# Kernel optimization log

Measured on AMD Instinct MI355X. Metric: run time of the kernel, lower is better.

Reference implementation:

```python
import jax, jax.numpy as jnp
import numpy as np

B, T, H, V = 16, 128, 512, 50257


def setup_inputs() -> dict:
    key = jax.random.key(0)
    ks = jax.random.split(key, 6)
    s = 0.05  # init_scale
    return {
        "tokens": jax.random.randint(ks[0], (B, T), 0, V, dtype=jnp.int32),
        "labels": jax.random.randint(ks[1], (B, T), 0, V, dtype=jnp.int32),
        "embedding": jax.random.normal(ks[2], (V, H), jnp.float32) * s,
        "W1": jax.random.normal(ks[3], (2 * H, 4 * H), jnp.float32) * s,
        "b1": jnp.zeros((4 * H,), jnp.float32),
        "W2": jax.random.normal(ks[4], (2 * H, 4 * H), jnp.float32) * s,
        "b2": jnp.zeros((4 * H,), jnp.float32),
        "softmax_w": jax.random.normal(ks[5], (H, V), jnp.float32) * s,
        "softmax_b": jnp.zeros((V,), jnp.float32),
    }


def _lstm_cell(x, h, c, W, b):
    # TF LSTMCell gate order: i, j (candidate), f, o; forget_bias = 0.0
    z = jnp.concatenate([x, h], axis=-1) @ W + b  # [B, 4H]
    i, j, f, o = jnp.split(z, 4, axis=-1)
    c_new = c * jax.nn.sigmoid(f) + jax.nn.sigmoid(i) * jnp.tanh(j)
    h_new = jnp.tanh(c_new) * jax.nn.sigmoid(o)
    return h_new, c_new


def _forward(tokens, labels, embedding, W1, b1, W2, b2, softmax_w, softmax_b):
    x = embedding[tokens]                 # [B, T, H] embedding lookup
    xs = jnp.swapaxes(x, 0, 1)            # [T, B, H] time-major for scan
    zeros = jnp.zeros((B, H), x.dtype)

    def step(carry, xt):
        c1, h1, c2, h2 = carry
        h1n, c1n = _lstm_cell(xt, h1, c1, W1, b1)
        h2n, c2n = _lstm_cell(h1n, h2, c2, W2, b2)
        return (c1n, h1n, c2n, h2n), h2n

    _, hs = jax.lax.scan(step, (zeros, zeros, zeros, zeros), xs)  # hs: [T, B, H]
    output = jnp.swapaxes(hs, 0, 1).reshape(-1, H)                # [B*T, H]
    logits = output @ softmax_w + softmax_b                       # [B*T, V]
    logp = jax.nn.log_softmax(logits, axis=-1)
    ll = jnp.take_along_axis(logp, labels.reshape(-1, 1), axis=1)[:, 0]
    cost = -jnp.sum(ll) / B  # sequence_loss_by_example summed, / batch_size
    return cost


def reference(tokens, labels, embedding, W1, b1, W2, b2, softmax_w, softmax_b):
    return _forward(tokens, labels, embedding, W1, b1, W2, b2, softmax_w, softmax_b)
```

## Files before the change

kernel.cpp:

```cpp
#include <hip/hip_runtime.h>

#define B_ 16
#define T_ 128
#define H_ 512
#define V_ 50257
#define VP_ 50304
#define NBLK 393
#define M_ (B_*T_)
#define N4H 2048
#define KH 512
#define NKB 16
#define FP_ 32
#define NTILES (NBLK * 16)
#define NWORK 224
#define NCHUNK (VP_ * 16 / 16)
#define HP_ 520

typedef __attribute__((ext_vector_type(8))) short short8;
typedef __attribute__((ext_vector_type(4))) float floatx4;
typedef unsigned long long u64;

static __device__ __forceinline__ unsigned short f2bf(float f) {
    unsigned int u = __builtin_bit_cast(unsigned int, f);
    unsigned int r = (u + 0x7FFFu + ((u >> 16) & 1u)) >> 16;
    return (unsigned short)r;
}
static __device__ __forceinline__ void st_ic(u64* p, u64 v) {
    __hip_atomic_store(p, v, __ATOMIC_RELAXED, __HIP_MEMORY_SCOPE_AGENT);
}

__global__ void k_init(const int* __restrict__ labels, int* __restrict__ lab_r,
                       unsigned short* __restrict__ zeroh, int* __restrict__ flags) {
    int tid = blockIdx.x * blockDim.x + threadIdx.x;
    if (tid < M_) {
        int t = tid >> 4, b = tid & 15;
        lab_r[tid] = labels[b * T_ + t];
    }
    if (tid < B_ * H_) zeroh[tid] = 0;
    if (tid < 34 * FP_) flags[tid] = 0;
}

__global__ void k_embed(const int* __restrict__ tokens, const float* __restrict__ emb,
                        unsigned short* __restrict__ X) {
    int tid = blockIdx.x * blockDim.x + threadIdx.x;
    if (tid >= M_ * H_) return;
    int row = tid >> 9, col = tid & 511;
    int t = row >> 4, b = row & 15;
    int tok = tokens[b * T_ + t];
    X[tid] = f2bf(emb[(size_t)tok * H_ + col]);
}

__global__ void k_pack(const float* __restrict__ src, int ld, int nvalid, int nkb,
                       int nchunks, unsigned short* __restrict__ dst) {
    int tid = blockIdx.x * blockDim.x + threadIdx.x;
    int lane = tid & 63, chunk = tid >> 6;
    if (chunk >= nchunks) return;
    int nt = chunk / nkb, kb = chunk % nkb;
    int n = nt * 16 + (lane & 15);
    int k = kb * 32 + ((lane >> 4) << 3);
    unsigned short vals[8];
    if (n < nvalid) {
#pragma unroll
        for (int j = 0; j < 8; ++j) vals[j] = f2bf(src[(size_t)(k + j) * ld + n]);
    } else {
#pragma unroll
        for (int j = 0; j < 8; ++j) vals[j] = 0;
    }
    *(short8*)(dst + (size_t)chunk * 512 + lane * 8) = *(short8*)vals;
}

__global__ __launch_bounds__(256, 2) void k_gemm_bias(
        const unsigned short* __restrict__ A, const unsigned short* __restrict__ Bp,
        const float* __restrict__ bias, float* __restrict__ C) {
    int bn = blockIdx.x, bm = blockIdx.y;
    int tid = threadIdx.x, lane = tid & 63, w = tid >> 6;
    int wm = w >> 1, wn = w & 1;
    int l15 = lane & 15, quad = lane >> 4;
    floatx4 acc[4][4];
#pragma unroll
    for (int i = 0; i < 4; ++i)
#pragma unroll
        for (int j = 0; j < 4; ++j) acc[i][j] = (floatx4){0.f, 0.f, 0.f, 0.f};
    const unsigned short* Abase = A + (size_t)(bm * 128 + wm * 64 + l15) * KH + quad * 8;
    int ntg0 = bn * 8 + wn * 4;
#pragma unroll 4
    for (int kb = 0; kb < NKB; ++kb) {
        short8 af[4], bf[4];
#pragma unroll
        for (int mt = 0; mt < 4; ++mt) af[mt] = *(const short8*)(Abase + mt * 16 * KH + kb * 32);
#pragma unroll
        for (int nt = 0; nt < 4; ++nt)
            bf[nt] = *(const short8*)(Bp + ((size_t)(ntg0 + nt) * NKB + kb) * 512 + lane * 8);
#pragma unroll
        for (int mt = 0; mt < 4; ++mt)
#pragma unroll
            for (int nt = 0; nt < 4; ++nt)
                acc[mt][nt] = __builtin_amdgcn_mfma_f32_16x16x32_bf16(af[mt], bf[nt], acc[mt][nt], 0, 0, 0);
    }
#pragma unroll
    for (int nt = 0; nt < 4; ++nt) {
        int col = bn * 128 + wn * 64 + nt * 16 + l15;
        float bv = bias[col];
#pragma unroll
        for (int mt = 0; mt < 4; ++mt) {
            int row0 = bm * 128 + wm * 64 + mt * 16 + quad * 4;
#pragma unroll
            for (int r = 0; r < 4; ++r)
                C[(size_t)(row0 + r) * N4H + col] = acc[mt][nt][r] + bv;
        }
    }
}

__global__ __launch_bounds__(512, 2) void k_mega(
        const float* __restrict__ Zpre1, const float* __restrict__ W1,
        const float* __restrict__ W2, const float* __restrict__ b2,
        const unsigned short* __restrict__ zeroh,
        unsigned short* __restrict__ H1, unsigned short* __restrict__ H2,
        int* __restrict__ flags,
        const float* __restrict__ sw, unsigned short* __restrict__ SWP,
        const float* __restrict__ sb, const int* __restrict__ lab_r,
        float* __restrict__ pm, float* __restrict__ ps, float* __restrict__ labv) {
    const int blk = blockIdx.x, tid = threadIdx.x;
    const int lane = tid & 63, w = tid >> 6;
    const int l15 = lane & 15, quad = lane >> 4;
    __shared__ unsigned short hs1[16 * HP_];
    __shared__ unsigned short hs2[16 * HP_];
    __shared__ float zs[128 * 17];
    u64* H1u = (u64*)H1;
    u64* H2u = (u64*)H2;

    if (blk < 32) {
        const bool isL2 = blk >= 16;
        const int bj = isL2 ? blk - 16 : blk;
        const int g = w >> 1, half = w & 1;
        const int nt = g * 32 + bj * 2 + half;
        const int colg = g * 512 + bj * 32 + half * 16 + l15;

        short8 bfr[32];
        {
            unsigned short vals[8];
            if (!isL2) {
#pragma unroll
                for (int kb = 0; kb < 16; ++kb) {
#pragma unroll
                    for (int j = 0; j < 8; ++j)
                        vals[j] = f2bf(W1[(size_t)(512 + kb * 32 + quad * 8 + j) * N4H + nt * 16 + l15]);
                    bfr[kb] = *(short8*)vals;
                }
            } else {
#pragma unroll
                for (int kb = 0; kb < 32; ++kb) {
#pragma unroll
                    for (int j = 0; j < 8; ++j)
                        vals[j] = f2bf(W2[(size_t)(kb * 32 + quad * 8 + j) * N4H + nt * 16 + l15]);
                    bfr[kb] = *(short8*)vals;
                }
            }
        }
        const float b2c = isL2 ? b2[colg] : 0.f;
        float creg = 0.f;

        for (int s = 0; s < T_; ++s) {
            float zpre[4];
            if (!isL2) {
#pragma unroll
                for (int r = 0; r < 4; ++r)
                    zpre[r] = Zpre1[(size_t)(s * 16 + quad * 4 + r) * N4H + colg];
            }
            if (w == 0 && (s > 0 || isL2)) {
                int tgt = 0x80000000;
                int* fp = flags;
                if (!isL2) {
                    if (lane < 16) { fp = flags + lane * FP_; tgt = s; }
                } else {
                    if (lane < 16) { fp = flags + lane * FP_; tgt = s + 1; }
                    else if (lane < 32) { fp = flags + lane * FP_; tgt = s; }
                }
                bool act = (!isL2 && lane < 16) || (isL2 && lane < 32);
                while (true) {
                    int v = act ? __hip_atomic_load(fp, __ATOMIC_RELAXED, __HIP_MEMORY_SCOPE_AGENT)
                                : 0x7fffffff;
                    if (__all(v >= tgt)) break;
                    __builtin_amdgcn_s_sleep(1);
                }
            }
            __syncthreads();

            if (!isL2) {
                const short8* src = (const short8*)((s == 0) ? zeroh
                                       : H1 + (size_t)(s - 1) * B_ * H_);
#pragma unroll
                for (int j = 0; j < 2; ++j) {
                    int idx = j * 512 + tid;
                    short8 v = src[idx];
                    *(short8*)(&hs1[(idx >> 6) * HP_ + (idx & 63) * 8]) = v;
                }
            } else {
                const short8* s1 = (const short8*)(H1 + (size_t)s * B_ * H_);
                const short8* s2 = (const short8*)((s == 0) ? zeroh
                                       : H2 + (size_t)(s - 1) * B_ * H_);
#pragma unroll
                for (int j = 0; j < 2; ++j) {
                    int idx = j * 512 + tid;
                    short8 v = s1[idx];
                    *(short8*)(&hs1[(idx >> 6) * HP_ + (idx & 63) * 8]) = v;
                }
#pragma unroll
                for (int j = 0; j < 2; ++j) {
                    int idx = j * 512 + tid;
                    short8 v = s2[idx];
                    *(short8*)(&hs2[(idx >> 6) * HP_ + (idx & 63) * 8]) = v;
                }
            }
            __syncthreads();

            if (!isL2) {
                floatx4 a0 = (floatx4){0.f,0.f,0.f,0.f}, a1 = (floatx4){0.f,0.f,0.f,0.f};
#pragma unroll
                for (int kb = 0; kb < 8; ++kb) {
                    short8 af = *(const short8*)(&hs1[l15 * HP_ + kb * 32 + quad * 8]);
                    a0 = __builtin_amdgcn_mfma_f32_16x16x32_bf16(af, bfr[kb], a0, 0, 0, 0);
                }
#pragma unroll
                for (int kb = 8; kb < 16; ++kb) {
                    short8 af = *(const short8*)(&hs1[l15 * HP_ + kb * 32 + quad * 8]);
                    a1 = __builtin_amdgcn_mfma_f32_16x16x32_bf16(af, bfr[kb], a1, 0, 0, 0);
                }
                const int zcol = g * 32 + half * 16 + l15;
#pragma unroll
                for (int r = 0; r < 4; ++r)
                    zs[zcol * 17 + quad * 4 + r] = a0[r] + a1[r] + zpre[r];
            } else {
                floatx4 a0 = (floatx4){0.f,0.f,0.f,0.f}, a1 = (floatx4){0.f,0.f,0.f,0.f};
#pragma unroll
                for (int kb = 0; kb < 16; ++kb) {
                    short8 af = *(const short8*)(&hs1[l15 * HP_ + kb * 32 + quad * 8]);
                    a0 = __builtin_amdgcn_mfma_f32_16x16x32_bf16(af, bfr[kb], a0, 0, 0, 0);
                }
#pragma unroll
                for (int kb = 0; kb < 16; ++kb) {
                    short8 af = *(const short8*)(&hs2[l15 * HP_ + kb * 32 + quad * 8]);
                    a1 = __builtin_amdgcn_mfma_f32_16x16x32_bf16(af, bfr[16 + kb], a1, 0, 0, 0);
                }
                const int zcol = g * 32 + half * 16 + l15;
#pragma unroll
                for (int r = 0; r < 4; ++r)
                    zs[zcol * 17 + quad * 4 + r] = a0[r] + a1[r] + b2c;
            }
            __syncthreads();

            {
                int u = tid >> 4, b = tid & 15;
                float zi = zs[(0 * 32 + u) * 17 + b];
                float zj = zs[(1 * 32 + u) * 17 + b];
                float zf = zs[(2 * 32 + u) * 17 + b];
                float zo = zs[(3 * 32 + u) * 17 + b];
                float si = 1.f / (1.f + __expf(-zi));
                float sf = 1.f / (1.f + __expf(-zf));
                float so = 1.f / (1.f + __expf(-zo));
                float cn = creg * sf + si * tanhf(zj);
                creg = cn;
                int hvi = (int)f2bf(tanhf(cn) * so);
                int lb = lane & 15;
                unsigned int h0 = (unsigned int)__shfl(hvi, lb);
                unsigned int h1v = (unsigned int)__shfl(hvi, lb + 16);
                unsigned int h2v = (unsigned int)__shfl(hvi, lb + 32);
                unsigned int h3v = (unsigned int)__shfl(hvi, lb + 48);
                if (lane < 16) {
                    u64 v = (u64)(h0 | (h1v << 16)) | ((u64)(h2v | (h3v << 16)) << 32);
                    u64* Hd = isL2 ? H2u : H1u;
                    st_ic(Hd + (size_t)(s * 16 + lane) * 128 + bj * 8 + w, v);
                }
            }
            __builtin_amdgcn_s_waitcnt(0x0F70);
            __syncthreads();
            if (tid == 0)
                __hip_atomic_store(flags + blk * FP_, s + 1, __ATOMIC_RELAXED,
                                   __HIP_MEMORY_SCOPE_AGENT);
        }
    } else {
        const int wid = blk - 32;
        int* wdone = flags + 32 * FP_;

        for (int t = 0; ; ++t) {
            int c = wid + NWORK * (8 * t + w);
            if (c >= NCHUNK) break;
            int cnt = c >> 4, ckb = c & 15;
            int n = cnt * 16 + l15;
            int kk = ckb * 32 + quad * 8;
            unsigned short vals[8];
            if (n < V_) {
#pragma unroll
                for (int j = 0; j < 8; ++j) vals[j] = f2bf(sw[(size_t)(kk + j) * V_ + n]);
            } else {
#pragma unroll
                for (int j = 0; j < 8; ++j) vals[j] = 0;
            }
            u64 v0 = (u64)vals[0] | ((u64)vals[1] << 16) | ((u64)vals[2] << 32) | ((u64)vals[3] << 48);
            u64 v1 = (u64)vals[4] | ((u64)vals[5] << 16) | ((u64)vals[6] << 32) | ((u64)vals[7] << 48);
            u64* dst = (u64*)(SWP + (size_t)c * 512 + lane * 8);
            st_ic(dst, v0);
            st_ic(dst + 1, v1);
        }
        __builtin_amdgcn_s_waitcnt(0x0F70);
        __syncthreads();
        if (tid == 0)
            __hip_atomic_fetch_add(wdone, 1, __ATOMIC_RELAXED, __HIP_MEMORY_SCOPE_AGENT);
        if (w == 0) {
            while (true) {
                int v = (lane == 0)
                    ? __hip_atomic_load(wdone, __ATOMIC_RELAXED, __HIP_MEMORY_SCOPE_AGENT)
                    : 0x7fffffff;
                if (__all(v >= NWORK)) break;
                __builtin_amdgcn_s_sleep(8);
            }
        }
        __syncthreads();

        int done_seen = 0;
        for (int k = wid; k < NTILES; k += NWORK) {
            int bm = k / NBLK, bn = k - bm * NBLK;
            int tgt = bm * 8 + 8;
            if (tgt > done_seen) {
                if (w == 0) {
                    int* fp = flags + (16 + (lane & 15)) * FP_;
                    while (true) {
                        int v = (lane < 16)
                            ? __hip_atomic_load(fp, __ATOMIC_RELAXED, __HIP_MEMORY_SCOPE_AGENT)
                            : 0x7fffffff;
                        if (__all(v >= tgt)) break;
                        __builtin_amdgcn_s_sleep(8);
                    }
                }
                __syncthreads();
                done_seen = tgt;
            }
            floatx4 acc[8];
#pragma unroll
            for (int j = 0; j < 8; ++j) acc[j] = (floatx4){0.f, 0.f, 0.f, 0.f};
            const short8* Abase = (const short8*)(H2 + (size_t)(bm * 128 + w * 16 + l15) * KH) + quad;
            int ntg0 = bn * 8;
#pragma unroll 4
            for (int kb = 0; kb < NKB; ++kb) {
                short8 af = Abase[kb * 4];
#pragma unroll
                for (int nt = 0; nt < 8; ++nt) {
                    short8 bf = *(const short8*)(SWP + ((size_t)(ntg0 + nt) * NKB + kb) * 512 + lane * 8);
                    acc[nt] = __builtin_amdgcn_mfma_f32_16x16x32_bf16(af, bf, acc[nt], 0, 0, 0);
                }
            }
            float bv[8]; int colg[8]; bool valid[8];
#pragma unroll
            for (int nt = 0; nt < 8; ++nt) {
                colg[nt] = bn * 128 + nt * 16 + l15;
                valid[nt] = colg[nt] < V_;
                bv[nt] = valid[nt] ? sb[colg[nt]] : 0.f;
            }
#pragma unroll
            for (int r = 0; r < 4; ++r) {
                float m = -3.0e38f;
#pragma unroll
                for (int nt = 0; nt < 8; ++nt) {
                    float v = valid[nt] ? acc[nt][r] + bv[nt] : -3.0e38f;
                    acc[nt][r] = v;
                    m = fmaxf(m, v);
                }
#pragma unroll
                for (int d = 1; d < 16; d <<= 1) m = fmaxf(m, __shfl_xor(m, d, 16));
                float sm = 0.f;
#pragma unroll
                for (int nt = 0; nt < 8; ++nt)
                    if (valid[nt]) sm += __expf(acc[nt][r] - m);
#pragma unroll
                for (int d = 1; d < 16; d <<= 1) sm += __shfl_xor(sm, d, 16);
                int rowg = bm * 128 + w * 16 + quad * 4 + r;
                int lc = lab_r[rowg];
#pragma unroll
                for (int nt = 0; nt < 8; ++nt)
                    if (valid[nt] && colg[nt] == lc) labv[rowg] = acc[nt][r];
                if (l15 == 0) {
                    pm[(size_t)rowg * NBLK + bn] = m;
                    ps[(size_t)rowg * NBLK + bn] = sm;
                }
            }
        }
    }
}

__global__ void k_rowreduce(const float* __restrict__ pm, const float* __restrict__ ps,
                            const float* __restrict__ labv, float* __restrict__ ll) {
    int row = blockIdx.x;
    int lane = threadIdx.x;
    const float* pmr = pm + (size_t)row * NBLK;
    const float* psr = ps + (size_t)row * NBLK;
    float m = -3.0e38f;
    for (int j = lane; j < NBLK; j += 64) m = fmaxf(m, pmr[j]);
#pragma unroll
    for (int d = 1; d < 64; d <<= 1) m = fmaxf(m, __shfl_xor(m, d, 64));
    float s = 0.f;
    for (int j = lane; j < NBLK; j += 64) s += psr[j] * __expf(pmr[j] - m);
#pragma unroll
    for (int d = 1; d < 64; d <<= 1) s += __shfl_xor(s, d, 64);
    if (lane == 0) ll[row] = labv[row] - m - logf(s);
}

__global__ void k_final(const float* __restrict__ ll, float* __restrict__ out) {
    int lane = threadIdx.x;
    float s = 0.f;
    for (int i = lane; i < M_; i += 64) s += ll[i];
#pragma unroll
    for (int d = 1; d < 64; d <<= 1) s += __shfl_xor(s, d, 64);
    if (lane == 0) out[0] = -s / (float)B_;
}

extern "C" void kernel_launch(void* const* d_in, const int* in_sizes, int n_in,
                              void* d_out, int out_size, void* d_ws, size_t ws_size,
                              hipStream_t stream) {
    const int* tokens = (const int*)d_in[0];
    const int* labels = (const int*)d_in[1];
    const float* emb = (const float*)d_in[2];
    const float* W1 = (const float*)d_in[3];
    const float* b1 = (const float*)d_in[4];
    const float* W2 = (const float*)d_in[5];
    const float* b2 = (const float*)d_in[6];
    const float* sw = (const float*)d_in[7];
    const float* sb = (const float*)d_in[8];
    float* out = (float*)d_out;

    char* ws = (char*)d_ws;
    size_t off = 0;
    auto alloc = [&](size_t bytes) {
        void* p = ws + off;
        off = (off + bytes + 255) & ~(size_t)255;
        return p;
    };
    unsigned short* X    = (unsigned short*)alloc((size_t)M_ * KH * 2);
    unsigned short* H1   = (unsigned short*)alloc((size_t)M_ * KH * 2);
    unsigned short* H2   = (unsigned short*)alloc((size_t)M_ * KH * 2);
    unsigned short* W1xP = (unsigned short*)alloc((size_t)N4H * KH * 2);
    unsigned short* SWP  = (unsigned short*)alloc((size_t)VP_ * KH * 2);
    float* Z     = (float*)alloc((size_t)M_ * N4H * 4);
    unsigned short* zeroh = (unsigned short*)alloc((size_t)B_ * H_ * 2);
    float* pm   = (float*)alloc((size_t)M_ * NBLK * 4);
    float* ps   = (float*)alloc((size_t)M_ * NBLK * 4);
    float* labv = (float*)alloc((size_t)M_ * 4);
    int*   lab_r = (int*)alloc((size_t)M_ * 4);
    float* ll   = (float*)alloc((size_t)M_ * 4);
    int*   flags = (int*)alloc((size_t)34 * FP_ * 4);

    k_init<<<64, 256, 0, stream>>>(labels, lab_r, zeroh, flags);
    k_embed<<<(M_ * H_) / 256, 256, 0, stream>>>(tokens, emb, X);
    k_pack<<<512, 256, 0, stream>>>(W1, N4H, N4H, 16, 2048, W1xP);

    k_gemm_bias<<<dim3(16, 16), 256, 0, stream>>>(X, W1xP, b1, Z);

    k_mega<<<256, 512, 0, stream>>>(Z, W1, W2, b2, zeroh, H1, H2, flags,
                                    sw, SWP, sb, lab_r, pm, ps, labv);

    k_rowreduce<<<M_, 64, 0, stream>>>(pm, ps, labv, ll);
    k_final<<<1, 64, 0, stream>>>(ll, out);
}
```

Measured before the change: 767.5 us.

## Replace flag barriers with step-tagged hidden-state words polled directly

Each hidden-state value is now stored as a 32-bit word that packs the bf16 value with a step tag. Consumer blocks poll their own slice of that data with cache-bypassing vector loads until every tag matches, which removes the separate flag write, the waitcnt-plus-barrier before signalling, and the flag poll on each recurrent step. Layer 2 keeps a double-buffered tagged slot and writes a flag only every 8 steps, for the downstream softmax workers. The step-0 matmuls are skipped and the three setup kernels are merged into one launch. In exchange, hidden-state traffic doubles and correctness now depends on the per-word tags, and therefore on stores landing atomically with their tags.

```diff
diff --git a/kernel.cpp b/kernel.cpp
--- a/kernel.cpp
+++ b/kernel.cpp
@@ -14,11 +14,13 @@
 #define NTILES (NBLK * 16)
 #define NWORK 224
 #define NCHUNK (VP_ * 16 / 16)
-#define HP_ 520
+#define HP_ 536
 
 typedef __attribute__((ext_vector_type(8))) short short8;
 typedef __attribute__((ext_vector_type(4))) float floatx4;
+typedef __attribute__((ext_vector_type(4))) unsigned int u32x4;
 typedef unsigned long long u64;
+typedef unsigned int u32;
 
 static __device__ __forceinline__ unsigned short f2bf(float f) {
     unsigned int u = __builtin_bit_cast(unsigned int, f);
@@ -28,45 +30,117 @@
 static __device__ __forceinline__ void st_ic(u64* p, u64 v) {
     __hip_atomic_store(p, v, __ATOMIC_RELAXED, __HIP_MEMORY_SCOPE_AGENT);
 }
-
-__global__ void k_init(const int* __restrict__ labels, int* __restrict__ lab_r,
-                       unsigned short* __restrict__ zeroh, int* __restrict__ flags) {
-    int tid = blockIdx.x * blockDim.x + threadIdx.x;
-    if (tid < M_) {
-        int t = tid >> 4, b = tid & 15;
-        lab_r[tid] = labels[b * T_ + t];
-    }
-    if (tid < B_ * H_) zeroh[tid] = 0;
-    if (tid < 34 * FP_) flags[tid] = 0;
-}
-
-__global__ void k_embed(const int* __restrict__ tokens, const float* __restrict__ emb,
-                        unsigned short* __restrict__ X) {
-    int tid = blockIdx.x * blockDim.x + threadIdx.x;
-    if (tid >= M_ * H_) return;
-    int row = tid >> 9, col = tid & 511;
-    int t = row >> 4, b = row & 15;
-    int tok = tokens[b * T_ + t];
-    X[tid] = f2bf(emb[(size_t)tok * H_ + col]);
-}
-
-__global__ void k_pack(const float* __restrict__ src, int ld, int nvalid, int nkb,
-                       int nchunks, unsigned short* __restrict__ dst) {
-    int tid = blockIdx.x * blockDim.x + threadIdx.x;
-    int lane = tid & 63, chunk = tid >> 6;
-    if (chunk >= nchunks) return;
-    int nt = chunk / nkb, kb = chunk % nkb;
-    int n = nt * 16 + (lane & 15);
-    int k = kb * 32 + ((lane >> 4) << 3);
-    unsigned short vals[8];
-    if (n < nvalid) {
-#pragma unroll
-        for (int j = 0; j < 8; ++j) vals[j] = f2bf(src[(size_t)(k + j) * ld + n]);
+static __device__ __forceinline__ void st_ic32(u32* p, u32 v) {
+    __hip_atomic_store(p, v, __ATOMIC_RELAXED, __HIP_MEMORY_SCOPE_AGENT);
+}
+
+static __device__ __forceinline__ void poll16(const u32* p, u32 tag, u32* v) {
+    u32x4 a0, a1, a2, a3;
+    while (true) {
+        asm volatile(
+            "global_load_dwordx4 %0, %4, off sc0 sc1\n\t"
+            "global_load_dwordx4 %1, %4, off offset:16 sc0 sc1\n\t"
+            "global_load_dwordx4 %2, %4, off offset:32 sc0 sc1\n\t"
+            "global_load_dwordx4 %3, %4, off offset:48 sc0 sc1\n\t"
+            "s_waitcnt vmcnt(0)"
+            : "=&v"(a0), "=&v"(a1), "=&v"(a2), "=&v"(a3)
+            : "v"(p)
+            : "memory");
+        u32 bad = 0;
+#pragma unroll
+        for (int j = 0; j < 4; ++j)
+            bad |= ((a0[j] ^ tag) & 0xffffu) | ((a1[j] ^ tag) & 0xffffu) |
+                   ((a2[j] ^ tag) & 0xffffu) | ((a3[j] ^ tag) & 0xffffu);
+        if (bad == 0) break;
+        __builtin_amdgcn_s_sleep(1);
+    }
+#pragma unroll
+    for (int j = 0; j < 4; ++j) { v[j] = a0[j]; v[4+j] = a1[j]; v[8+j] = a2[j]; v[12+j] = a3[j]; }
+}
+
+static __device__ __forceinline__ void poll2(const u32* p1, u32 tag1,
+                                             const u32* p2, u32 tag2,
+                                             u32* v1, u32* v2) {
+    u32x4 a0, a1, a2, a3, b0, b1, b2, b3;
+    while (true) {
+        asm volatile(
+            "global_load_dwordx4 %0, %8, off sc0 sc1\n\t"
+            "global_load_dwordx4 %1, %8, off offset:16 sc0 sc1\n\t"
+            "global_load_dwordx4 %2, %8, off offset:32 sc0 sc1\n\t"
+            "global_load_dwordx4 %3, %8, off offset:48 sc0 sc1\n\t"
+            "global_load_dwordx4 %4, %9, off sc0 sc1\n\t"
+            "global_load_dwordx4 %5, %9, off offset:16 sc0 sc1\n\t"
+            "global_load_dwordx4 %6, %9, off offset:32 sc0 sc1\n\t"
+            "global_load_dwordx4 %7, %9, off offset:48 sc0 sc1\n\t"
+            "s_waitcnt vmcnt(0)"
+            : "=&v"(a0), "=&v"(a1), "=&v"(a2), "=&v"(a3),
+              "=&v"(b0), "=&v"(b1), "=&v"(b2), "=&v"(b3)
+            : "v"(p1), "v"(p2)
+            : "memory");
+        u32 bad = 0;
+#pragma unroll
+        for (int j = 0; j < 4; ++j) {
+            bad |= ((a0[j] ^ tag1) & 0xffffu) | ((a1[j] ^ tag1) & 0xffffu) |
+                   ((a2[j] ^ tag1) & 0xffffu) | ((a3[j] ^ tag1) & 0xffffu);
+            bad |= ((b0[j] ^ tag2) & 0xffffu) | ((b1[j] ^ tag2) & 0xffffu) |
+                   ((b2[j] ^ tag2) & 0xffffu) | ((b3[j] ^ tag2) & 0xffffu);
+        }
+        if (bad == 0) break;
+        __builtin_amdgcn_s_sleep(1);
+    }
+#pragma unroll
+    for (int j = 0; j < 4; ++j) {
+        v1[j] = a0[j]; v1[4+j] = a1[j]; v1[8+j] = a2[j]; v1[12+j] = a3[j];
+        v2[j] = b0[j]; v2[4+j] = b1[j]; v2[8+j] = b2[j]; v2[12+j] = b3[j];
+    }
+}
+
+static __device__ __forceinline__ void stage_row(unsigned short* hs, int tid, const u32* v) {
+    int b = tid >> 5, c0 = (tid & 31) << 4;
+    u32x4 w0, w1;
+#pragma unroll
+    for (int i = 0; i < 4; ++i) w0[i] = (v[2*i]   >> 16) | (v[2*i+1]   & 0xffff0000u);
+#pragma unroll
+    for (int i = 0; i < 4; ++i) w1[i] = (v[8+2*i] >> 16) | (v[8+2*i+1] & 0xffff0000u);
+    *(u32x4*)(hs + (size_t)b * HP_ + c0)     = w0;
+    *(u32x4*)(hs + (size_t)b * HP_ + c0 + 8) = w1;
+}
+
+__global__ void k_setup(const int* __restrict__ tokens, const int* __restrict__ labels,
+                        const float* __restrict__ emb, const float* __restrict__ W1,
+                        unsigned short* __restrict__ X, unsigned short* __restrict__ W1xP,
+                        u32* __restrict__ T1, u32* __restrict__ T2,
+                        int* __restrict__ lab_r, int* __restrict__ flags) {
+    int blk = blockIdx.x, t = threadIdx.x;
+    if (blk < 4096) {
+        int tid = blk * 256 + t;
+        int row = tid >> 9, col = tid & 511;
+        int tt = row >> 4, b = row & 15;
+        int tok = tokens[b * T_ + tt];
+        X[tid] = f2bf(emb[(size_t)tok * H_ + col]);
+    } else if (blk < 4608) {
+        int chunk = (blk - 4096) * 4 + (t >> 6);
+        int lane = t & 63;
+        int nt = chunk >> 4, kb = chunk & 15;
+        int n = nt * 16 + (lane & 15);
+        int k = kb * 32 + ((lane >> 4) << 3);
+        unsigned short vals[8];
+#pragma unroll
+        for (int j = 0; j < 8; ++j) vals[j] = f2bf(W1[(size_t)(k + j) * N4H + n]);
+        *(short8*)(W1xP + (size_t)chunk * 512 + lane * 8) = *(short8*)vals;
+    } else if (blk < 5120) {
+        u32x4 z = (u32x4){0, 0, 0, 0};
+        u32x4* p = (u32x4*)T1 + (size_t)(blk - 4608) * 512 + t * 2;
+        p[0] = z; p[1] = z;
+    } else if (blk < 5128) {
+        u32x4 z = (u32x4){0, 0, 0, 0};
+        u32x4* p = (u32x4*)T2 + (size_t)(blk - 5120) * 512 + t * 2;
+        p[0] = z; p[1] = z;
+    } else if (blk == 5128) {
+        for (int i = t; i < M_; i += 256) { int tt = i >> 4, b = i & 15; lab_r[i] = labels[b * T_ + tt]; }
     } else {
-#pragma unroll
-        for (int j = 0; j < 8; ++j) vals[j] = 0;
-    }
-    *(short8*)(dst + (size_t)chunk * 512 + lane * 8) = *(short8*)vals;
+        for (int i = t; i < 34 * FP_; i += 256) flags[i] = 0;
+    }
 }
 
 __global__ __launch_bounds__(256, 2) void k_gemm_bias(
@@ -114,9 +188,8 @@
 __global__ __launch_bounds__(512, 2) void k_mega(
         const float* __restrict__ Zpre1, const float* __restrict__ W1,
         const float* __restrict__ W2, const float* __restrict__ b2,
-        const unsigned short* __restrict__ zeroh,
-        unsigned short* __restrict__ H1, unsigned short* __restrict__ H2,
-        int* __restrict__ flags,
+        u32* __restrict__ T1, u32* __restrict__ T2,
+        unsigned short* __restrict__ H2, int* __restrict__ flags,
         const float* __restrict__ sw, unsigned short* __restrict__ SWP,
         const float* __restrict__ sb, const int* __restrict__ lab_r,
         float* __restrict__ pm, float* __restrict__ ps, float* __restrict__ labv) {
@@ -126,7 +199,6 @@
     __shared__ unsigned short hs1[16 * HP_];
     __shared__ unsigned short hs2[16 * HP_];
     __shared__ float zs[128 * 17];
-    u64* H1u = (u64*)H1;
     u64* H2u = (u64*)H2;
 
     if (blk < 32) {
@@ -159,6 +231,8 @@
         }
         const float b2c = isL2 ? b2[colg] : 0.f;
         float creg = 0.f;
+        const int pu = tid >> 4, pb = tid & 15;
+        u32* Tself = isL2 ? T2 : T1;
 
         for (int s = 0; s < T_; ++s) {
             float zpre[4];
@@ -167,64 +241,38 @@
                 for (int r = 0; r < 4; ++r)
                     zpre[r] = Zpre1[(size_t)(s * 16 + quad * 4 + r) * N4H + colg];
             }
-            if (w == 0 && (s > 0 || isL2)) {
-                int tgt = 0x80000000;
-                int* fp = flags;
-                if (!isL2) {
-                    if (lane < 16) { fp = flags + lane * FP_; tgt = s; }
+            u32 v1[16], v2[16];
+            if (!isL2) {
+                if (s > 0) {
+                    poll16(T1 + (size_t)(s - 1) * 8192 + tid * 16, (u32)s, v1);
+                    stage_row(hs1, tid, v1);
+                }
+            } else {
+                if (s == 0) {
+                    poll16(T1 + (size_t)tid * 16, 1u, v1);
+                    stage_row(hs1, tid, v1);
                 } else {
-                    if (lane < 16) { fp = flags + lane * FP_; tgt = s + 1; }
-                    else if (lane < 32) { fp = flags + lane * FP_; tgt = s; }
-                }
-                bool act = (!isL2 && lane < 16) || (isL2 && lane < 32);
-                while (true) {
-                    int v = act ? __hip_atomic_load(fp, __ATOMIC_RELAXED, __HIP_MEMORY_SCOPE_AGENT)
-                                : 0x7fffffff;
-                    if (__all(v >= tgt)) break;
-                    __builtin_amdgcn_s_sleep(1);
-                }
-            }
-            __syncthreads();
-
-            if (!isL2) {
-                const short8* src = (const short8*)((s == 0) ? zeroh
-                                       : H1 + (size_t)(s - 1) * B_ * H_);
-#pragma unroll
-                for (int j = 0; j < 2; ++j) {
-                    int idx = j * 512 + tid;
-                    short8 v = src[idx];
-                    *(short8*)(&hs1[(idx >> 6) * HP_ + (idx & 63) * 8]) = v;
-                }
-            } else {
-                const short8* s1 = (const short8*)(H1 + (size_t)s * B_ * H_);
-                const short8* s2 = (const short8*)((s == 0) ? zeroh
-                                       : H2 + (size_t)(s - 1) * B_ * H_);
-#pragma unroll
-                for (int j = 0; j < 2; ++j) {
-                    int idx = j * 512 + tid;
-                    short8 v = s1[idx];
-                    *(short8*)(&hs1[(idx >> 6) * HP_ + (idx & 63) * 8]) = v;
-                }
-#pragma unroll
-                for (int j = 0; j < 2; ++j) {
-                    int idx = j * 512 + tid;
-                    short8 v = s2[idx];
-                    *(short8*)(&hs2[(idx >> 6) * HP_ + (idx & 63) * 8]) = v;
+                    poll2(T1 + (size_t)s * 8192 + tid * 16, (u32)(s + 1),
+                          T2 + (size_t)((s - 1) & 1) * 8192 + tid * 16, (u32)s, v1, v2);
+                    stage_row(hs1, tid, v1);
+                    stage_row(hs2, tid, v2);
                 }
             }
             __syncthreads();
 
             if (!isL2) {
                 floatx4 a0 = (floatx4){0.f,0.f,0.f,0.f}, a1 = (floatx4){0.f,0.f,0.f,0.f};
-#pragma unroll
-                for (int kb = 0; kb < 8; ++kb) {
-                    short8 af = *(const short8*)(&hs1[l15 * HP_ + kb * 32 + quad * 8]);
-                    a0 = __builtin_amdgcn_mfma_f32_16x16x32_bf16(af, bfr[kb], a0, 0, 0, 0);
-                }
-#pragma unroll
-                for (int kb = 8; kb < 16; ++kb) {
-                    short8 af = *(const short8*)(&hs1[l15 * HP_ + kb * 32 + quad * 8]);
-                    a1 = __builtin_amdgcn_mfma_f32_16x16x32_bf16(af, bfr[kb], a1, 0, 0, 0);
+                if (s > 0) {
+#pragma unroll
+                    for (int kb = 0; kb < 8; ++kb) {
+                        short8 af = *(const short8*)(&hs1[l15 * HP_ + kb * 32 + quad * 8]);
+                        a0 = __builtin_amdgcn_mfma_f32_16x16x32_bf16(af, bfr[kb], a0, 0, 0, 0);
+                    }
+#pragma unroll
+                    for (int kb = 8; kb < 16; ++kb) {
+                        short8 af = *(const short8*)(&hs1[l15 * HP_ + kb * 32 + quad * 8]);
+                        a1 = __builtin_amdgcn_mfma_f32_16x16x32_bf16(af, bfr[kb], a1, 0, 0, 0);
+                    }
                 }
                 const int zcol = g * 32 + half * 16 + l15;
 #pragma unroll
@@ -237,10 +285,12 @@
                     short8 af = *(const short8*)(&hs1[l15 * HP_ + kb * 32 + quad * 8]);
                     a0 = __builtin_amdgcn_mfma_f32_16x16x32_bf16(af, bfr[kb], a0, 0, 0, 0);
                 }
-#pragma unroll
-                for (int kb = 0; kb < 16; ++kb) {
-                    short8 af = *(const short8*)(&hs2[l15 * HP_ + kb * 32 + quad * 8]);
-                    a1 = __builtin_amdgcn_mfma_f32_16x16x32_bf16(af, bfr[16 + kb], a1, 0, 0, 0);
+                if (s > 0) {
+#pragma unroll
+                    for (int kb = 0; kb < 16; ++kb) {
+                        short8 af = *(const short8*)(&hs2[l15 * HP_ + kb * 32 + quad * 8]);
+                        a1 = __builtin_amdgcn_mfma_f32_16x16x32_bf16(af, bfr[16 + kb], a1, 0, 0, 0);
+                    }
                 }
                 const int zcol = g * 32 + half * 16 + l15;
 #pragma unroll
@@ -250,33 +300,39 @@
             __syncthreads();
 
             {
-                int u = tid >> 4, b = tid & 15;
-                float zi = zs[(0 * 32 + u) * 17 + b];
-                float zj = zs[(1 * 32 + u) * 17 + b];
-                float zf = zs[(2 * 32 + u) * 17 + b];
-                float zo = zs[(3 * 32 + u) * 17 + b];
+                float zi = zs[(0 * 32 + pu) * 17 + pb];
+                float zj = zs[(1 * 32 + pu) * 17 + pb];
+                float zf = zs[(2 * 32 + pu) * 17 + pb];
+                float zo = zs[(3 * 32 + pu) * 17 + pb];
                 float si = 1.f / (1.f + __expf(-zi));
                 float sf = 1.f / (1.f + __expf(-zf));
                 float so = 1.f / (1.f + __expf(-zo));
                 float cn = creg * sf + si * tanhf(zj);
                 creg = cn;
-                int hvi = (int)f2bf(tanhf(cn) * so);
-                int lb = lane & 15;
-                unsigned int h0 = (unsigned int)__shfl(hvi, lb);
-                unsigned int h1v = (unsigned int)__shfl(hvi, lb + 16);
-                unsigned int h2v = (unsigned int)__shfl(hvi, lb + 32);
-                unsigned int h3v = (unsigned int)__shfl(hvi, lb + 48);
-                if (lane < 16) {
-                    u64 v = (u64)(h0 | (h1v << 16)) | ((u64)(h2v | (h3v << 16)) << 32);
-                    u64* Hd = isL2 ? H2u : H1u;
-                    st_ic(Hd + (size_t)(s * 16 + lane) * 128 + bj * 8 + w, v);
-                }
-            }
-            __builtin_amdgcn_s_waitcnt(0x0F70);
-            __syncthreads();
-            if (tid == 0)
-                __hip_atomic_store(flags + blk * FP_, s + 1, __ATOMIC_RELAXED,
-                                   __HIP_MEMORY_SCOPE_AGENT);
+                unsigned short hbf = f2bf(tanhf(cn) * so);
+                u32 tv = ((u32)hbf << 16) | (u32)(s + 1);
+                size_t slot = isL2 ? (size_t)(s & 1) * 8192 : (size_t)s * 8192;
+                st_ic32(Tself + slot + pb * 512 + bj * 32 + pu, tv);
+                if (isL2) {
+                    int hvi = (int)hbf;
+                    int lb = lane & 15;
+                    unsigned int h0  = (unsigned int)__shfl(hvi, lb);
+                    unsigned int h1v = (unsigned int)__shfl(hvi, lb + 16);
+                    unsigned int h2v = (unsigned int)__shfl(hvi, lb + 32);
+                    unsigned int h3v = (unsigned int)__shfl(hvi, lb + 48);
+                    if (lane < 16) {
+                        u64 vv = (u64)(h0 | (h1v << 16)) | ((u64)(h2v | (h3v << 16)) << 32);
+                        st_ic(H2u + (size_t)(s * 16 + lane) * 128 + bj * 8 + w, vv);
+                    }
+                }
+            }
+            if (isL2 && ((s & 7) == 7)) {
+                __builtin_amdgcn_s_waitcnt(0x0F70);
+                __syncthreads();
+                if (tid == 0)
+                    __hip_atomic_store(flags + blk * FP_, s + 1, __ATOMIC_RELAXED,
+                                       __HIP_MEMORY_SCOPE_AGENT);
+            }
         }
     } else {
         const int wid = blk - 32;
@@ -435,12 +491,12 @@
         return p;
     };
     unsigned short* X    = (unsigned short*)alloc((size_t)M_ * KH * 2);
-    unsigned short* H1   = (unsigned short*)alloc((size_t)M_ * KH * 2);
     unsigned short* H2   = (unsigned short*)alloc((size_t)M_ * KH * 2);
     unsigned short* W1xP = (unsigned short*)alloc((size_t)N4H * KH * 2);
     unsigned short* SWP  = (unsigned short*)alloc((size_t)VP_ * KH * 2);
     float* Z     = (float*)alloc((size_t)M_ * N4H * 4);
-    unsigned short* zeroh = (unsigned short*)alloc((size_t)B_ * H_ * 2);
+    u32*   T1    = (u32*)alloc((size_t)T_ * B_ * H_ * 4);
+    u32*   T2    = (u32*)alloc((size_t)2 * B_ * H_ * 4);
     float* pm   = (float*)alloc((size_t)M_ * NBLK * 4);
     float* ps   = (float*)alloc((size_t)M_ * NBLK * 4);
     float* labv = (float*)alloc((size_t)M_ * 4);
@@ -448,13 +504,11 @@
     float* ll   = (float*)alloc((size_t)M_ * 4);
     int*   flags = (int*)alloc((size_t)34 * FP_ * 4);
 
-    k_init<<<64, 256, 0, stream>>>(labels, lab_r, zeroh, flags);
-    k_embed<<<(M_ * H_) / 256, 256, 0, stream>>>(tokens, emb, X);
-    k_pack<<<512, 256, 0, stream>>>(W1, N4H, N4H, 16, 2048, W1xP);
+    k_setup<<<5130, 256, 0, stream>>>(tokens, labels, emb, W1, X, W1xP, T1, T2, lab_r, flags);
 
     k_gemm_bias<<<dim3(16, 16), 256, 0, stream>>>(X, W1xP, b1, Z);
 
-    k_mega<<<256, 512, 0, stream>>>(Z, W1, W2, b2, zeroh, H1, H2, flags,
+    k_mega<<<256, 512, 0, stream>>>(Z, W1, W2, b2, T1, T2, H2, flags,
                                     sw, SWP, sb, lab_r, pm, ps, labv);
 
     k_rowreduce<<<M_, 64, 0, stream>>>(pm, ps, labv, ll);
```

Result: slower. 855.4 us (+11.5%).
